# Performance work log

Measured on AMD Instinct MI355X. Metric: run time of the kernel, lower is better.

Reference implementation:

```python
import jax, jax.numpy as jnp
import numpy as np

STRIDE = (1, 1)
PADDING = (1, 1)


def setup_inputs() -> dict:
    key = jax.random.key(0)
    k1, k2, k3 = jax.random.split(key, 3)
    x = jax.random.normal(k1, (32, 128, 56, 56), dtype=jnp.float32)
    # xavier_uniform for weight (out, in, kh, kw): bound = sqrt(6/(fan_in+fan_out))
    fan_in = 128 * 3 * 3
    fan_out = 256 * 3 * 3
    bound = float(np.sqrt(6.0 / (fan_in + fan_out)))
    weight = jax.random.uniform(k2, (256, 128, 3, 3), dtype=jnp.float32,
                                minval=-bound, maxval=bound)
    bias = jax.random.normal(k3, (256,), dtype=jnp.float32)
    return {"x": x, "weight": weight, "bias": bias}


def reference(x, weight, bias):
    # Faithful cross-correlation conv (torch semantics): NCHW input, OIHW weight.
    out = jax.lax.conv_general_dilated(
        x, weight,
        window_strides=STRIDE,
        padding=[(PADDING[0], PADDING[0]), (PADDING[1], PADDING[1])],
        dimension_numbers=("NCHW", "OIHW", "NCHW"),
    )
    out = out + bias[None, :, None, None]
    return out
```

## Files before the change

kernel.cpp:

```cpp
#include <hip/hip_runtime.h>
#include <cstdint>

typedef __bf16 bf16_t;
typedef __bf16 bf16x8 __attribute__((ext_vector_type(8)));
typedef float  f32x4  __attribute__((ext_vector_type(4)));

#define XPAD_ELEMS (32UL*58*58*128)
#define WPERM_OFF  (XPAD_ELEMS*2)
#define WPERM_ELEMS (256UL*9*128)
#define WS_NEEDED  (WPERM_OFF + WPERM_ELEMS*2)

__device__ __forceinline__ void async16(const bf16_t* g, const bf16_t* l) {
  __builtin_amdgcn_global_load_lds(
      (const __attribute__((address_space(1))) void*)g,
      (__attribute__((address_space(3))) void*)l, 16, 0, 0);
}

__global__ __launch_bounds__(256) void k_xform(const float* __restrict__ x, bf16_t* __restrict__ Xp) {
  const int b = blockIdx.x;
  const int n = b / 58, hp = b % 58;
  bf16_t* drow = Xp + ((size_t)n * 58 + hp) * 58 * 128;
  const int t = threadIdx.x;
  uint4 z; z.x = z.y = z.z = z.w = 0;
  if (hp == 0 || hp == 57) {
    uint4* p = (uint4*)drow;
    for (int i = t; i < 928; i += 256) p[i] = z;
    return;
  }
  if (t < 32) {
    uint4* p0 = (uint4*)drow;
    uint4* p1 = (uint4*)(drow + 57 * 128);
    if (t < 16) p0[t] = z; else p1[t - 16] = z;
  }
  const int h = hp - 1;
  const float* src = x + (size_t)n * 401408 + h * 56;
  __shared__ float lds[128 * 57];
  for (int i = t; i < 7168; i += 256) {
    int c = i / 56;
    int w = i - c * 56;
    lds[c * 57 + w] = src[(size_t)c * 3136 + w];
  }
  __syncthreads();
  bf16_t* dst = drow + 128;
  for (int i = t; i < 3584; i += 256) {
    int cp = i & 63, w = i >> 6;
    int c0 = cp * 2;
    unsigned short u0 = __builtin_bit_cast(unsigned short, (bf16_t)lds[c0 * 57 + w]);
    unsigned short u1 = __builtin_bit_cast(unsigned short, (bf16_t)lds[(c0 + 1) * 57 + w]);
    *(unsigned int*)(dst + (size_t)w * 128 + c0) = (unsigned)u0 | ((unsigned)u1 << 16);
  }
}

__global__ void k_wperm(const float* __restrict__ wt, bf16_t* __restrict__ Wp) {
  int i = blockIdx.x * 256 + threadIdx.x;
  if (i >= 294912) return;
  int e  = i & 7;
  int o  = (i >> 3) & 255;
  int kc = (i >> 11) & 3;
  int t  = i >> 13;
  int ci = t & 3, rs = t >> 2;
  int c  = ci * 32 + kc * 8 + e;
  Wp[i] = (bf16_t)wt[o * 1152 + c * 9 + rs];
}

__global__ void k_naive(const float* __restrict__ x, const float* __restrict__ wt,
                        const float* __restrict__ bs, float* __restrict__ out) {
  int idx = blockIdx.x * 256 + threadIdx.x;
  if (idx >= 25690112) return;
  int w = idx % 56; int tmp = idx / 56;
  int h = tmp % 56; tmp /= 56;
  int k = tmp % 256; int n = tmp / 256;
  float acc = bs[k];
  for (int c = 0; c < 128; ++c)
    for (int r = 0; r < 3; ++r) {
      int hy = h + r - 1; if ((unsigned)hy >= 56u) continue;
      for (int s = 0; s < 3; ++s) {
        int wx = w + s - 1; if ((unsigned)wx >= 56u) continue;
        acc += x[((size_t)(n * 128 + c) * 56 + hy) * 56 + wx] *
               wt[((size_t)(k * 128 + c) * 3 + r) * 3 + s];
      }
    }
  out[idx] = acc;
}

__global__ __launch_bounds__(256, 2) void k_conv(const bf16_t* __restrict__ Xp,
                                                 const bf16_t* __restrict__ Wpk,
                                                 const float* __restrict__ bias,
                                                 float* __restrict__ out) {
  __shared__ bf16_t strip[3712 * 8];
  const int tid = threadIdx.x, lane = tid & 63, wv = tid >> 6;
  const int sid = (int)blockIdx.x;
  const int n   = sid / 28;
  const int h0  = (sid - n * 28) * 2;

  const bf16_t* xrow = Xp + ((size_t)n * 58 + h0) * 58 * 128;
#pragma unroll
  for (int r = 0; r < 14; ++r) {
    int slot = r * 256 + tid;
    int pix = slot >> 4, cp = slot & 15;
    int hp = pix / 58, wp = pix - hp * 58;
    int cl = cp ^ (wp & 7);
    async16(xrow + ((size_t)(hp * 58 + wp)) * 128 + cl * 8,
            strip + (r * 256 + wv * 64) * 8);
  }
  if (tid < 128) {
    int slot = 3584 + tid;
    int pix = slot >> 4, cp = slot & 15;
    int hp = pix / 58, wp = pix - hp * 58;
    int cl = cp ^ (wp & 7);
    async16(xrow + ((size_t)(hp * 58 + wp)) * 128 + cl * 8,
            strip + (3584 + wv * 64) * 8);
  }

  const int fr = lane & 15, fg = lane >> 4;
  int pixoff[7];
#pragma unroll
  for (int ni = 0; ni < 7; ++ni) {
    int pq = ni * 16 + fr;
    int oh = (pq >= 56) ? 1 : 0;
    pixoff[ni] = (pq + 2 * oh) * 128;
  }

  const bf16_t* wsrc = Wpk + fg * 2048 + (wv * 64 + fr) * 8;
  bf16x8 areg[2][4];
#pragma unroll
  for (int mi = 0; mi < 4; ++mi) {
    areg[0][mi] = *(const bf16x8*)(wsrc + mi * 128);
    areg[1][mi] = *(const bf16x8*)(wsrc + 8192 + mi * 128);
  }

#define BBASE(t) ((((((t) >> 2) / 3) * 58 + ((t) >> 2) % 3) * 16 +                 \
                   ((((t) & 3) * 4 + fg) ^ ((fr + ((t) >> 2) % 3) & 7))) * 8)

  __syncthreads();

  f32x4 acc[4][7] = {};
  bf16x8 bcur[7], bnxt[7];
#pragma unroll
  for (int ni = 0; ni < 7; ++ni)
    bcur[ni] = *(const bf16x8*)&strip[pixoff[ni] + BBASE(0)];

#pragma unroll
  for (int t = 0; t < 36; ++t) {
    const int pb = t & 1;
    if (t + 1 < 36) {
      const int nb = BBASE(t + 1);
#pragma unroll
      for (int ni = 0; ni < 7; ++ni)
        bnxt[ni] = *(const bf16x8*)&strip[pixoff[ni] + nb];
    }
    __builtin_amdgcn_s_setprio(1);
#pragma unroll
    for (int mi = 0; mi < 4; ++mi)
#pragma unroll
      for (int ni = 0; ni < 7; ++ni)
        acc[mi][ni] = __builtin_amdgcn_mfma_f32_16x16x32_bf16(areg[pb][mi], bcur[ni], acc[mi][ni], 0, 0, 0);
    __builtin_amdgcn_s_setprio(0);
    if (t + 2 < 36) {
#pragma unroll
      for (int mi = 0; mi < 4; ++mi)
        areg[pb][mi] = *(const bf16x8*)(wsrc + (size_t)(t + 2) * 8192 + mi * 128);
    }
#pragma unroll
    for (int ni = 0; ni < 7; ++ni)
      bcur[ni] = bnxt[ni];
  }
#undef BBASE

  const int mbase = wv * 64;
  float bv[4][4];
#pragma unroll
  for (int mi = 0; mi < 4; ++mi)
#pragma unroll
    for (int j = 0; j < 4; ++j)
      bv[mi][j] = bias[mbase + mi * 16 + fg * 4 + j];

#pragma unroll
  for (int ni = 0; ni < 7; ++ni) {
    int pq = ni * 16 + fr;
    int oh = (pq >= 56) ? 1 : 0;
    int ow = pq - oh * 56;
    int h = h0 + oh;
    float* ob = out + (size_t)n * 802816 + h * 56 + ow;
#pragma unroll
    for (int mi = 0; mi < 4; ++mi) {
      int kb = mbase + mi * 16 + fg * 4;
#pragma unroll
      for (int j = 0; j < 4; ++j)
        ob[(size_t)(kb + j) * 3136] = acc[mi][ni][j] + bv[mi][j];
    }
  }
}

extern "C" void kernel_launch(void* const* d_in, const int* in_sizes, int n_in,
                              void* d_out, int out_size, void* d_ws, size_t ws_size,
                              hipStream_t stream) {
  const float* x  = (const float*)d_in[0];
  const float* wt = (const float*)d_in[1];
  const float* bs = (const float*)d_in[2];
  float* out = (float*)d_out;

  if (ws_size < WS_NEEDED) {
    k_naive<<<(25690112 + 255) / 256, 256, 0, stream>>>(x, wt, bs, out);
    return;
  }

  bf16_t* Xp  = (bf16_t*)d_ws;
  bf16_t* Wpk = (bf16_t*)((char*)d_ws + WPERM_OFF);

  k_xform<<<1856, 256, 0, stream>>>(x, Xp);
  k_wperm<<<1152, 256, 0, stream>>>(wt, Wpk);
  k_conv <<<896, 256, 0, stream>>>(Xp, Wpk, bs, out);
}
```

Measured before the change: 78.63 us.

## Fuse input NCHW-to-bf16 transform and padding into the conv kernel

Removes the separate k_xform pass that wrote a padded NHWC bf16 copy of the input to workspace. Each conv block now reads its four fp32 input rows directly from NCHW in 16-channel slices, stages them in an LDS temp buffer, and converts and packs them into the swizzled bf16 strip, handling padding inline. This drops a full global write and re-read of the transformed input. In exchange, the strip load is now synchronous with 16 barriers per block, each input row is read by two blocks, and the extra LDS buffer may lower occupancy.

```diff
diff --git a/kernel.cpp b/kernel.cpp
--- a/kernel.cpp
+++ b/kernel.cpp
@@ -5,51 +5,8 @@
 typedef __bf16 bf16x8 __attribute__((ext_vector_type(8)));
 typedef float  f32x4  __attribute__((ext_vector_type(4)));
 
-#define XPAD_ELEMS (32UL*58*58*128)
-#define WPERM_OFF  (XPAD_ELEMS*2)
 #define WPERM_ELEMS (256UL*9*128)
-#define WS_NEEDED  (WPERM_OFF + WPERM_ELEMS*2)
-
-__device__ __forceinline__ void async16(const bf16_t* g, const bf16_t* l) {
-  __builtin_amdgcn_global_load_lds(
-      (const __attribute__((address_space(1))) void*)g,
-      (__attribute__((address_space(3))) void*)l, 16, 0, 0);
-}
-
-__global__ __launch_bounds__(256) void k_xform(const float* __restrict__ x, bf16_t* __restrict__ Xp) {
-  const int b = blockIdx.x;
-  const int n = b / 58, hp = b % 58;
-  bf16_t* drow = Xp + ((size_t)n * 58 + hp) * 58 * 128;
-  const int t = threadIdx.x;
-  uint4 z; z.x = z.y = z.z = z.w = 0;
-  if (hp == 0 || hp == 57) {
-    uint4* p = (uint4*)drow;
-    for (int i = t; i < 928; i += 256) p[i] = z;
-    return;
-  }
-  if (t < 32) {
-    uint4* p0 = (uint4*)drow;
-    uint4* p1 = (uint4*)(drow + 57 * 128);
-    if (t < 16) p0[t] = z; else p1[t - 16] = z;
-  }
-  const int h = hp - 1;
-  const float* src = x + (size_t)n * 401408 + h * 56;
-  __shared__ float lds[128 * 57];
-  for (int i = t; i < 7168; i += 256) {
-    int c = i / 56;
-    int w = i - c * 56;
-    lds[c * 57 + w] = src[(size_t)c * 3136 + w];
-  }
-  __syncthreads();
-  bf16_t* dst = drow + 128;
-  for (int i = t; i < 3584; i += 256) {
-    int cp = i & 63, w = i >> 6;
-    int c0 = cp * 2;
-    unsigned short u0 = __builtin_bit_cast(unsigned short, (bf16_t)lds[c0 * 57 + w]);
-    unsigned short u1 = __builtin_bit_cast(unsigned short, (bf16_t)lds[(c0 + 1) * 57 + w]);
-    *(unsigned int*)(dst + (size_t)w * 128 + c0) = (unsigned)u0 | ((unsigned)u1 << 16);
-  }
-}
+#define WS_NEEDED  (WPERM_ELEMS*2)
 
 __global__ void k_wperm(const float* __restrict__ wt, bf16_t* __restrict__ Wp) {
   int i = blockIdx.x * 256 + threadIdx.x;
@@ -83,36 +40,66 @@
   out[idx] = acc;
 }
 
-__global__ __launch_bounds__(256, 2) void k_conv(const bf16_t* __restrict__ Xp,
+__global__ __launch_bounds__(256, 2) void k_conv(const float* __restrict__ x,
                                                  const bf16_t* __restrict__ Wpk,
                                                  const float* __restrict__ bias,
                                                  float* __restrict__ out) {
   __shared__ bf16_t strip[3712 * 8];
+  __shared__ float  tmp[16 * 4 * 58];
   const int tid = threadIdx.x, lane = tid & 63, wv = tid >> 6;
   const int sid = (int)blockIdx.x;
   const int n   = sid / 28;
   const int h0  = (sid - n * 28) * 2;
 
-  const bf16_t* xrow = Xp + ((size_t)n * 58 + h0) * 58 * 128;
+  const int fr = lane & 15, fg = lane >> 4;
+
+  const bf16_t* wsrc = Wpk + fg * 2048 + ((wv << 6) + fr) * 8;
+  bf16x8 areg[2][4];
 #pragma unroll
-  for (int r = 0; r < 14; ++r) {
-    int slot = r * 256 + tid;
-    int pix = slot >> 4, cp = slot & 15;
-    int hp = pix / 58, wp = pix - hp * 58;
-    int cl = cp ^ (wp & 7);
-    async16(xrow + ((size_t)(hp * 58 + wp)) * 128 + cl * 8,
-            strip + (r * 256 + wv * 64) * 8);
-  }
-  if (tid < 128) {
-    int slot = 3584 + tid;
-    int pix = slot >> 4, cp = slot & 15;
-    int hp = pix / 58, wp = pix - hp * 58;
-    int cl = cp ^ (wp & 7);
-    async16(xrow + ((size_t)(hp * 58 + wp)) * 128 + cl * 8,
-            strip + (3584 + wv * 64) * 8);
+  for (int mi = 0; mi < 4; ++mi) {
+    areg[0][mi] = *(const bf16x8*)(wsrc + mi * 128);
+    areg[1][mi] = *(const bf16x8*)(wsrc + 8192 + mi * 128);
   }
 
-  const int fr = lane & 15, fg = lane >> 4;
+  const float* xs = x + (size_t)n * 401408;
+  const int cw = tid >> 6, wl = tid & 63;
+  for (int s = 0; s < 8; ++s) {
+#pragma unroll
+    for (int k = 0; k < 16; ++k) {
+      int cr = k * 4 + cw;
+      int c = cr >> 2, r = cr & 3;
+      int h_in = h0 + r - 1;
+      float v = 0.f;
+      if (((unsigned)h_in < 56u) & (wl < 56))
+        v = xs[(size_t)(s * 16 + c) * 3136 + h_in * 56 + wl];
+      if (wl < 56) tmp[(c * 4 + r) * 58 + wl] = v;
+    }
+    __syncthreads();
+#pragma unroll
+    for (int rd = 0; rd < 2; ++rd) {
+      int slot = rd * 256 + tid;
+      if (slot < 464) {
+        int half = slot & 1, pix = slot >> 1;
+        int hp = pix / 58, wp = pix - hp * 58;
+        int cl = s * 2 + half;
+        int cp = cl ^ (wp & 7);
+        unsigned pk0 = 0, pk1 = 0, pk2 = 0, pk3 = 0;
+        if (wp >= 1 && wp <= 56) {
+          const float* tb = &tmp[(half * 8) * 4 * 58 + hp * 58 + (wp - 1)];
+          unsigned u[8];
+#pragma unroll
+          for (int e = 0; e < 8; ++e)
+            u[e] = (unsigned)__builtin_bit_cast(unsigned short, (bf16_t)tb[e * 4 * 58]);
+          pk0 = u[0] | (u[1] << 16); pk1 = u[2] | (u[3] << 16);
+          pk2 = u[4] | (u[5] << 16); pk3 = u[6] | (u[7] << 16);
+        }
+        uint4 uq; uq.x = pk0; uq.y = pk1; uq.z = pk2; uq.w = pk3;
+        *(uint4*)&strip[((size_t)pix * 16 + cp) * 8] = uq;
+      }
+    }
+    __syncthreads();
+  }
+
   int pixoff[7];
 #pragma unroll
   for (int ni = 0; ni < 7; ++ni) {
@@ -121,18 +108,8 @@
     pixoff[ni] = (pq + 2 * oh) * 128;
   }
 
-  const bf16_t* wsrc = Wpk + fg * 2048 + (wv * 64 + fr) * 8;
-  bf16x8 areg[2][4];
-#pragma unroll
-  for (int mi = 0; mi < 4; ++mi) {
-    areg[0][mi] = *(const bf16x8*)(wsrc + mi * 128);
-    areg[1][mi] = *(const bf16x8*)(wsrc + 8192 + mi * 128);
-  }
-
 #define BBASE(t) ((((((t) >> 2) / 3) * 58 + ((t) >> 2) % 3) * 16 +                 \
                    ((((t) & 3) * 4 + fg) ^ ((fr + ((t) >> 2) % 3) & 7))) * 8)
-
-  __syncthreads();
 
   f32x4 acc[4][7] = {};
   bf16x8 bcur[7], bnxt[7];
@@ -205,10 +182,8 @@
     return;
   }
 
-  bf16_t* Xp  = (bf16_t*)d_ws;
-  bf16_t* Wpk = (bf16_t*)((char*)d_ws + WPERM_OFF);
+  bf16_t* Wpk = (bf16_t*)d_ws;
 
-  k_xform<<<1856, 256, 0, stream>>>(x, Xp);
   k_wperm<<<1152, 256, 0, stream>>>(wt, Wpk);
-  k_conv <<<896, 256, 0, stream>>>(Xp, Wpk, bs, out);
+  k_conv <<<896, 256, 0, stream>>>(x, Wpk, bs, out);
 }
```

New measurement: 120.5 us. 1.53x slower.
